# Kernel tuning notes

Measured on AMD Instinct MI355X. Metric: run time of the kernel, lower is better.

## Reference

```python
import jax, jax.numpy as jnp
import numpy as np

N_NODES = 100_000
N_EDGES = 1_600_000
HIDDEN = 128
OUT_DIM = 400


def setup_inputs() -> dict:
    key = jax.random.key(0)
    ks = jax.random.split(key, 6)
    x = jax.random.normal(ks[0], (N_NODES, 1), dtype=jnp.float32)
    edge_index = jax.random.randint(ks[1], (2, N_EDGES), 0, N_NODES, dtype=jnp.int32)
    # Glorot-style init for the two GCN weight matrices
    W1 = jax.random.normal(ks[2], (1, HIDDEN), dtype=jnp.float32) * (1.0 / np.sqrt(1 + HIDDEN))
    b1 = jnp.zeros((HIDDEN,), dtype=jnp.float32)
    W2 = jax.random.normal(ks[3], (HIDDEN, OUT_DIM), dtype=jnp.float32) * (1.0 / np.sqrt(HIDDEN + OUT_DIM))
    b2 = jnp.zeros((OUT_DIM,), dtype=jnp.float32)
    return {"x": x, "edge_index": edge_index, "W1": W1, "b1": b1, "W2": W2, "b2": b2}


def _gcn_layer(x, W, b, row, col, norm, num_nodes):
    # PyG GCNConv: out[col] += norm * (x @ W)[row]; then + bias
    h = x @ W                                   # [N, F_out]
    msg = h[row] * norm[:, None]                # [E+N, F_out] gather + scale
    out = jax.ops.segment_sum(msg, col, num_segments=num_nodes)  # scatter-add
    return out + b


def reference(x, edge_index, W1, b1, W2, b2):
    n = x.shape[0]
    loops = jnp.arange(n, dtype=edge_index.dtype)
    row = jnp.concatenate([edge_index[0], loops])  # sources (+ self loops)
    col = jnp.concatenate([edge_index[1], loops])  # destinations (+ self loops)
    # symmetric normalization: deg over destinations, norm = d^-1/2[row] * d^-1/2[col]
    deg = jnp.zeros((n,), dtype=x.dtype).at[col].add(1.0)  # >=1 due to self loops
    dinv = jax.lax.rsqrt(deg)
    norm = dinv[row] * dinv[col]
    h = jax.nn.relu(_gcn_layer(x, W1, b1, row, col, norm, n))
    h = _gcn_layer(h, W2, b2, row, col, norm, n)
    return h.mean(axis=0)  # [OUT_DIM]
```

## Files before the change

kernel.cpp:

```cpp
#include <hip/hip_runtime.h>
#include <math.h>


constexpr int BKT_BITS = 10;
constexpr int BKT_SIZE = 1 << BKT_BITS;
constexpr int NBMAX    = 128;
constexpr int CAP      = 17408;
constexpr int SLICES   = 8;
constexpr int SLICES_D = 8;
constexpr int EPT      = 8;

__global__ void init_cur(int* __restrict__ curC, int* __restrict__ curR,
                         float* __restrict__ total) {
    int t = threadIdx.x;
    if (t < NBMAX) { curC[t] = t * CAP; curR[t] = t * CAP; }
    if (t < 128) total[t] = 0.0f;
}

__global__ void scatter_edges(const int* __restrict__ row, const int* __restrict__ col,
                              int* __restrict__ SC, int* __restrict__ SR,
                              int* __restrict__ curC, int* __restrict__ curR, int E) {
    __shared__ int hC[NBMAX], hR[NBMAX], bC[NBMAX], bR[NBMAX];
    const int TILE = blockDim.x * EPT;
    const int myBase = blockIdx.x * TILE + threadIdx.x * EPT;
    int r[EPT], c[EPT];
    if (myBase + EPT <= E) {
        int4 r0 = *reinterpret_cast<const int4*>(row + myBase);
        int4 r1 = *reinterpret_cast<const int4*>(row + myBase + 4);
        int4 c0 = *reinterpret_cast<const int4*>(col + myBase);
        int4 c1 = *reinterpret_cast<const int4*>(col + myBase + 4);
        r[0]=r0.x; r[1]=r0.y; r[2]=r0.z; r[3]=r0.w;
        r[4]=r1.x; r[5]=r1.y; r[6]=r1.z; r[7]=r1.w;
        c[0]=c0.x; c[1]=c0.y; c[2]=c0.z; c[3]=c0.w;
        c[4]=c1.x; c[5]=c1.y; c[6]=c1.z; c[7]=c1.w;
    } else {
#pragma unroll
        for (int j = 0; j < EPT; ++j) {
            int e = myBase + j;
            r[j] = (e < E) ? row[e] : -1;
            c[j] = (e < E) ? col[e] : -1;
        }
    }
    if (threadIdx.x < NBMAX) { hC[threadIdx.x] = 0; hR[threadIdx.x] = 0; }
    __syncthreads();
#pragma unroll
    for (int j = 0; j < EPT; ++j) {
        if (r[j] >= 0) {
            atomicAdd(&hC[c[j] >> BKT_BITS], 1);
            atomicAdd(&hR[r[j] >> BKT_BITS], 1);
        }
    }
    __syncthreads();
    if (threadIdx.x < NBMAX) {
        bC[threadIdx.x] = atomicAdd(&curC[threadIdx.x], hC[threadIdx.x]);
        hC[threadIdx.x] = 0;
        bR[threadIdx.x] = atomicAdd(&curR[threadIdx.x], hR[threadIdx.x]);
        hR[threadIdx.x] = 0;
    }
    __syncthreads();
#pragma unroll
    for (int j = 0; j < EPT; ++j) {
        if (r[j] >= 0) {
            int kb = c[j] >> BKT_BITS;
            int idx = bC[kb] + atomicAdd(&hC[kb], 1);
            if (idx < (kb + 1) * CAP)
                SC[idx] = ((c[j] & (BKT_SIZE - 1)) << 17) | r[j];
            int kb2 = r[j] >> BKT_BITS;
            int idx2 = bR[kb2] + atomicAdd(&hR[kb2], 1);
            if (idx2 < (kb2 + 1) * CAP)
                SR[idx2] = ((r[j] & (BKT_SIZE - 1)) << 17) | c[j];
        }
    }
}

__global__ void hist_deg(const int* __restrict__ SC, const int* __restrict__ cur,
                         float* __restrict__ P, int stride) {
    __shared__ float bins[BKT_SIZE];
    const int b = blockIdx.x / SLICES_D, s = blockIdx.x % SLICES_D;
    const int base = b * CAP;
    int len = cur[b] - base;
    len = len < CAP ? len : CAP;
    const int lo = base + (int)((long long)len * s / SLICES_D);
    const int hi = base + (int)((long long)len * (s + 1) / SLICES_D);
    for (int i = threadIdx.x; i < BKT_SIZE; i += blockDim.x) bins[i] = 0.0f;
    __syncthreads();
    for (int e = lo + threadIdx.x; e < hi; e += blockDim.x)
        atomicAdd(&bins[SC[e] >> 17], 1.0f);
    __syncthreads();
    float* dst = P + (size_t)s * stride + b * BKT_SIZE;
    for (int i = threadIdx.x; i < BKT_SIZE; i += blockDim.x) dst[i] = bins[i];
}

__global__ void finalize_deg(const float* __restrict__ Pd, const float* __restrict__ x,
                             float* __restrict__ dinv, float* __restrict__ u,
                             int N, int stride) {
    int i = blockIdx.x * blockDim.x + threadIdx.x;
    if (i >= N) return;
    float d = 1.0f;
#pragma unroll
    for (int s = 0; s < SLICES_D; ++s) d += Pd[(size_t)s * stride + i];
    float di = rsqrtf(d);
    dinv[i] = di;
    u[i] = di * x[i];
}

__global__ void hist_gather_both(const int* __restrict__ SC, const int* __restrict__ SR,
                                 const int* __restrict__ curC, const int* __restrict__ curR,
                                 const float* __restrict__ u, const float* __restrict__ dinv,
                                 float* __restrict__ Ps, float* __restrict__ Pw,
                                 int stride, int half) {
    __shared__ float bins[BKT_SIZE];
    const bool isW = blockIdx.x >= half;
    const int id = isW ? blockIdx.x - half : blockIdx.x;
    const int* S = isW ? SR : SC;
    const int* cur = isW ? curR : curC;
    const float* val = isW ? dinv : u;
    float* P = isW ? Pw : Ps;
    const int b = id / SLICES, s = id % SLICES;
    const int base = b * CAP;
    int len = cur[b] - base;
    len = len < CAP ? len : CAP;
    const int lo = base + (int)((long long)len * s / SLICES);
    const int hi = base + (int)((long long)len * (s + 1) / SLICES);
    for (int i = threadIdx.x; i < BKT_SIZE; i += blockDim.x) bins[i] = 0.0f;
    __syncthreads();
    for (int e = lo + threadIdx.x; e < hi; e += blockDim.x) {
        int v = S[e];
        atomicAdd(&bins[v >> 17], val[v & 0x1FFFF]);
    }
    __syncthreads();
    float* dst = P + (size_t)s * stride + b * BKT_SIZE;
    for (int i = threadIdx.x; i < BKT_SIZE; i += blockDim.x) dst[i] = bins[i];
}

__global__ void fused_node(const float* __restrict__ Ps, const float* __restrict__ Pw,
                           const float* __restrict__ dinv, const float* __restrict__ x,
                           const float* __restrict__ W1, const float* __restrict__ b1,
                           float* __restrict__ total, int N, int stride) {
    __shared__ float scs[256];
    __shared__ float ws[256];
    __shared__ float red[256];
    const int tid = threadIdx.x;
    const int i = blockIdx.x * 256 + tid;
    float scv = 0.0f, wv = 0.0f;
    if (i < N) {
        float sr = 0.0f, wr = 0.0f;
#pragma unroll
        for (int s = 0; s < SLICES; ++s) {
            sr += Ps[(size_t)s * stride + i];
            wr += Pw[(size_t)s * stride + i];
        }
        float di = dinv[i];
        scv = di * sr + di * di * x[i];
        wv  = di * (wr + di);
    }
    scs[tid] = scv;
    ws[tid]  = wv;
    __syncthreads();
    const int k = tid & 127;
    const int base = (tid >> 7) * 128;
    const float w1k = W1[k];
    const float b1k = b1[k];
    float acc = 0.0f;
#pragma unroll 4
    for (int j = 0; j < 128; ++j) {
        float h = scs[base + j] * w1k + b1k;
        h = h > 0.0f ? h : 0.0f;
        acc += ws[base + j] * h;
    }
    red[tid] = acc;
    __syncthreads();
    if (tid < 128)
        atomicAdd(&total[k], red[tid] + red[tid + 128]);
}

__global__ void final_out(const float* __restrict__ total,
                          const float* __restrict__ W2, const float* __restrict__ b2,
                          float* __restrict__ out, int OUT, float invN) {
    __shared__ float t[128];
    const int tid = threadIdx.x;
    if (tid < 128) t[tid] = total[tid] * invN;
    __syncthreads();
    const int d = blockIdx.x * 128 + tid;
    if (d < OUT) {
        float acc = b2[d];
#pragma unroll 4
        for (int kk = 0; kk < 128; ++kk) acc += t[kk] * W2[kk * OUT + d];
        out[d] = acc;
    }
}

extern "C" void kernel_launch(void* const* d_in, const int* in_sizes, int n_in,
                              void* d_out, int out_size, void* d_ws, size_t ws_size,
                              hipStream_t stream) {
    const float* x          = (const float*)d_in[0];
    const int*   edge_index = (const int*)  d_in[1];
    const float* W1         = (const float*)d_in[2];
    const float* b1         = (const float*)d_in[3];
    const float* W2         = (const float*)d_in[4];
    const float* b2         = (const float*)d_in[5];
    float* out = (float*)d_out;

    const int N   = in_sizes[0];
    const int E   = in_sizes[1] / 2;
    const int OUT = in_sizes[5];

    const int* row = edge_index;
    const int* col = edge_index + E;

    const int NB = (N + BKT_SIZE - 1) >> BKT_BITS;
    const int stride = NB * BKT_SIZE;

    char* p = (char*)d_ws;
    float* dinv  = (float*)p; p += (size_t)N * 4;
    float* u     = (float*)p; p += (size_t)N * 4;
    float* total = (float*)p; p += 512;
    int*   ints  = (int*)p;   p += 1024;
    int*   SC    = (int*)p;   p += (size_t)NB * CAP * 4;
    int*   SR    = (int*)p;   p += (size_t)NB * CAP * 4;
    float* P     = (float*)p;
    float* Ps    = P;
    float* Pw    = P + (size_t)SLICES * stride;

    int* curC = ints;
    int* curR = ints + NBMAX;

    const int TILE = 256 * EPT;
    const int nTiles = (E + TILE - 1) / TILE;

    init_cur<<<1, 256, 0, stream>>>(curC, curR, total);
    scatter_edges<<<nTiles, 256, 0, stream>>>(row, col, SC, SR, curC, curR, E);
    hist_deg<<<NB * SLICES_D, 256, 0, stream>>>(SC, curC, P, stride);
    finalize_deg<<<(N + 255) / 256, 256, 0, stream>>>(P, x, dinv, u, N, stride);
    const int half = NB * SLICES;
    hist_gather_both<<<2 * half, 256, 0, stream>>>(SC, SR, curC, curR, u, dinv,
                                                   Ps, Pw, stride, half);
    fused_node<<<(N + 255) / 256, 256, 0, stream>>>(Ps, Pw, dinv, x, W1, b1,
                                                    total, N, stride);
    final_out<<<(OUT + 127) / 128, 128, 0, stream>>>(total, W2, b2, out, OUT,
                                                     1.0f / (float)N);
}
```

Before: 168.9 us.

## Fuse GCN pipeline into one cooperative persistent kernel with grid syncs

Replaces the six separate kernel launches with a single cooperative kernel of 512 persistent blocks that runs each stage in grid-stride loops, separated by grid.sync(). Histogram stages now give each bucket to one block, with vectorised int4 reads, instead of splitting it into 8 slices with partial buffers, so the slice reduction passes are gone. The aim is to remove per-launch overhead and partial-sum traffic. The costs are grid-wide barrier latency and less parallelism in the histogram stages, since there are only about 98 buckets per pass (about 196 tasks in the combined gather stage), well below 512 blocks.

```diff
diff --git a/kernel.cpp b/kernel.cpp
--- a/kernel.cpp
+++ b/kernel.cpp
@@ -1,242 +1,248 @@
 #include <hip/hip_runtime.h>
+#include <hip/hip_cooperative_groups.h>
 #include <math.h>
+
+namespace cg = cooperative_groups;
 
 
 constexpr int BKT_BITS = 10;
 constexpr int BKT_SIZE = 1 << BKT_BITS;
-constexpr int NBMAX    = 128;
+constexpr int NBP      = 128;
 constexpr int CAP      = 17408;
-constexpr int SLICES   = 8;
-constexpr int SLICES_D = 8;
 constexpr int EPT      = 8;
+constexpr int TPB      = 256;
+constexpr int GRID     = 512;
 
 __global__ void init_cur(int* __restrict__ curC, int* __restrict__ curR,
                          float* __restrict__ total) {
     int t = threadIdx.x;
-    if (t < NBMAX) { curC[t] = t * CAP; curR[t] = t * CAP; }
+    if (t < NBP) { curC[t] = t * CAP; curR[t] = t * CAP; }
     if (t < 128) total[t] = 0.0f;
 }
 
-__global__ void scatter_edges(const int* __restrict__ row, const int* __restrict__ col,
-                              int* __restrict__ SC, int* __restrict__ SR,
-                              int* __restrict__ curC, int* __restrict__ curR, int E) {
-    __shared__ int hC[NBMAX], hR[NBMAX], bC[NBMAX], bR[NBMAX];
-    const int TILE = blockDim.x * EPT;
-    const int myBase = blockIdx.x * TILE + threadIdx.x * EPT;
-    int r[EPT], c[EPT];
-    if (myBase + EPT <= E) {
-        int4 r0 = *reinterpret_cast<const int4*>(row + myBase);
-        int4 r1 = *reinterpret_cast<const int4*>(row + myBase + 4);
-        int4 c0 = *reinterpret_cast<const int4*>(col + myBase);
-        int4 c1 = *reinterpret_cast<const int4*>(col + myBase + 4);
-        r[0]=r0.x; r[1]=r0.y; r[2]=r0.z; r[3]=r0.w;
-        r[4]=r1.x; r[5]=r1.y; r[6]=r1.z; r[7]=r1.w;
-        c[0]=c0.x; c[1]=c0.y; c[2]=c0.z; c[3]=c0.w;
-        c[4]=c1.x; c[5]=c1.y; c[6]=c1.z; c[7]=c1.w;
-    } else {
+__global__ __launch_bounds__(TPB, 4)
+void gcn_mono(const int* __restrict__ row, const int* __restrict__ col,
+              const float* __restrict__ x,
+              const float* __restrict__ W1, const float* __restrict__ b1,
+              const float* __restrict__ W2, const float* __restrict__ b2,
+              int* __restrict__ SC, int* __restrict__ SR,
+              int* __restrict__ curC, int* __restrict__ curR,
+              float* __restrict__ dinv, float* __restrict__ u,
+              float* __restrict__ s_raw, float* __restrict__ w_raw,
+              float* __restrict__ total, float* __restrict__ out,
+              int N, int E, int NB, int OUT) {
+    cg::grid_group grid = cg::this_grid();
+    __shared__ int hC[NBP], hR[NBP], bC[NBP], bR[NBP];
+    __shared__ float bins[BKT_SIZE];
+    __shared__ float scs[TPB], ws[TPB], red[TPB];
+    const int tid = threadIdx.x;
+
+    const int TILE = TPB * EPT;
+    const int nTiles = (E + TILE - 1) / TILE;
+    for (int t = blockIdx.x; t < nTiles; t += gridDim.x) {
+        const int myBase = t * TILE + tid * EPT;
+        int r[EPT], c[EPT];
+        if (myBase + EPT <= E) {
+            int4 r0 = *reinterpret_cast<const int4*>(row + myBase);
+            int4 r1 = *reinterpret_cast<const int4*>(row + myBase + 4);
+            int4 c0 = *reinterpret_cast<const int4*>(col + myBase);
+            int4 c1 = *reinterpret_cast<const int4*>(col + myBase + 4);
+            r[0]=r0.x; r[1]=r0.y; r[2]=r0.z; r[3]=r0.w;
+            r[4]=r1.x; r[5]=r1.y; r[6]=r1.z; r[7]=r1.w;
+            c[0]=c0.x; c[1]=c0.y; c[2]=c0.z; c[3]=c0.w;
+            c[4]=c1.x; c[5]=c1.y; c[6]=c1.z; c[7]=c1.w;
+        } else {
+#pragma unroll
+            for (int j = 0; j < EPT; ++j) {
+                int e = myBase + j;
+                r[j] = (e < E) ? row[e] : -1;
+                c[j] = (e < E) ? col[e] : -1;
+            }
+        }
+        if (tid < NBP) { hC[tid] = 0; hR[tid] = 0; }
+        __syncthreads();
 #pragma unroll
         for (int j = 0; j < EPT; ++j) {
-            int e = myBase + j;
-            r[j] = (e < E) ? row[e] : -1;
-            c[j] = (e < E) ? col[e] : -1;
-        }
-    }
-    if (threadIdx.x < NBMAX) { hC[threadIdx.x] = 0; hR[threadIdx.x] = 0; }
-    __syncthreads();
+            if (r[j] >= 0) {
+                atomicAdd(&hC[c[j] >> BKT_BITS], 1);
+                atomicAdd(&hR[r[j] >> BKT_BITS], 1);
+            }
+        }
+        __syncthreads();
+        if (tid < NBP) {
+            bC[tid] = atomicAdd(&curC[tid], hC[tid]);
+            hC[tid] = 0;
+            bR[tid] = atomicAdd(&curR[tid], hR[tid]);
+            hR[tid] = 0;
+        }
+        __syncthreads();
 #pragma unroll
-    for (int j = 0; j < EPT; ++j) {
-        if (r[j] >= 0) {
-            atomicAdd(&hC[c[j] >> BKT_BITS], 1);
-            atomicAdd(&hR[r[j] >> BKT_BITS], 1);
-        }
-    }
-    __syncthreads();
-    if (threadIdx.x < NBMAX) {
-        bC[threadIdx.x] = atomicAdd(&curC[threadIdx.x], hC[threadIdx.x]);
-        hC[threadIdx.x] = 0;
-        bR[threadIdx.x] = atomicAdd(&curR[threadIdx.x], hR[threadIdx.x]);
-        hR[threadIdx.x] = 0;
-    }
-    __syncthreads();
-#pragma unroll
-    for (int j = 0; j < EPT; ++j) {
-        if (r[j] >= 0) {
-            int kb = c[j] >> BKT_BITS;
-            int idx = bC[kb] + atomicAdd(&hC[kb], 1);
-            if (idx < (kb + 1) * CAP)
-                SC[idx] = ((c[j] & (BKT_SIZE - 1)) << 17) | r[j];
-            int kb2 = r[j] >> BKT_BITS;
-            int idx2 = bR[kb2] + atomicAdd(&hR[kb2], 1);
-            if (idx2 < (kb2 + 1) * CAP)
-                SR[idx2] = ((r[j] & (BKT_SIZE - 1)) << 17) | c[j];
-        }
-    }
-}
-
-__global__ void hist_deg(const int* __restrict__ SC, const int* __restrict__ cur,
-                         float* __restrict__ P, int stride) {
-    __shared__ float bins[BKT_SIZE];
-    const int b = blockIdx.x / SLICES_D, s = blockIdx.x % SLICES_D;
-    const int base = b * CAP;
-    int len = cur[b] - base;
-    len = len < CAP ? len : CAP;
-    const int lo = base + (int)((long long)len * s / SLICES_D);
-    const int hi = base + (int)((long long)len * (s + 1) / SLICES_D);
-    for (int i = threadIdx.x; i < BKT_SIZE; i += blockDim.x) bins[i] = 0.0f;
-    __syncthreads();
-    for (int e = lo + threadIdx.x; e < hi; e += blockDim.x)
-        atomicAdd(&bins[SC[e] >> 17], 1.0f);
-    __syncthreads();
-    float* dst = P + (size_t)s * stride + b * BKT_SIZE;
-    for (int i = threadIdx.x; i < BKT_SIZE; i += blockDim.x) dst[i] = bins[i];
-}
-
-__global__ void finalize_deg(const float* __restrict__ Pd, const float* __restrict__ x,
-                             float* __restrict__ dinv, float* __restrict__ u,
-                             int N, int stride) {
-    int i = blockIdx.x * blockDim.x + threadIdx.x;
-    if (i >= N) return;
-    float d = 1.0f;
-#pragma unroll
-    for (int s = 0; s < SLICES_D; ++s) d += Pd[(size_t)s * stride + i];
-    float di = rsqrtf(d);
-    dinv[i] = di;
-    u[i] = di * x[i];
-}
-
-__global__ void hist_gather_both(const int* __restrict__ SC, const int* __restrict__ SR,
-                                 const int* __restrict__ curC, const int* __restrict__ curR,
-                                 const float* __restrict__ u, const float* __restrict__ dinv,
-                                 float* __restrict__ Ps, float* __restrict__ Pw,
-                                 int stride, int half) {
-    __shared__ float bins[BKT_SIZE];
-    const bool isW = blockIdx.x >= half;
-    const int id = isW ? blockIdx.x - half : blockIdx.x;
-    const int* S = isW ? SR : SC;
-    const int* cur = isW ? curR : curC;
-    const float* val = isW ? dinv : u;
-    float* P = isW ? Pw : Ps;
-    const int b = id / SLICES, s = id % SLICES;
-    const int base = b * CAP;
-    int len = cur[b] - base;
-    len = len < CAP ? len : CAP;
-    const int lo = base + (int)((long long)len * s / SLICES);
-    const int hi = base + (int)((long long)len * (s + 1) / SLICES);
-    for (int i = threadIdx.x; i < BKT_SIZE; i += blockDim.x) bins[i] = 0.0f;
-    __syncthreads();
-    for (int e = lo + threadIdx.x; e < hi; e += blockDim.x) {
-        int v = S[e];
-        atomicAdd(&bins[v >> 17], val[v & 0x1FFFF]);
-    }
-    __syncthreads();
-    float* dst = P + (size_t)s * stride + b * BKT_SIZE;
-    for (int i = threadIdx.x; i < BKT_SIZE; i += blockDim.x) dst[i] = bins[i];
-}
-
-__global__ void fused_node(const float* __restrict__ Ps, const float* __restrict__ Pw,
-                           const float* __restrict__ dinv, const float* __restrict__ x,
-                           const float* __restrict__ W1, const float* __restrict__ b1,
-                           float* __restrict__ total, int N, int stride) {
-    __shared__ float scs[256];
-    __shared__ float ws[256];
-    __shared__ float red[256];
-    const int tid = threadIdx.x;
-    const int i = blockIdx.x * 256 + tid;
-    float scv = 0.0f, wv = 0.0f;
-    if (i < N) {
-        float sr = 0.0f, wr = 0.0f;
-#pragma unroll
-        for (int s = 0; s < SLICES; ++s) {
-            sr += Ps[(size_t)s * stride + i];
-            wr += Pw[(size_t)s * stride + i];
-        }
-        float di = dinv[i];
-        scv = di * sr + di * di * x[i];
-        wv  = di * (wr + di);
-    }
-    scs[tid] = scv;
-    ws[tid]  = wv;
-    __syncthreads();
+        for (int j = 0; j < EPT; ++j) {
+            if (r[j] >= 0) {
+                int kb = c[j] >> BKT_BITS;
+                int idx = bC[kb] + atomicAdd(&hC[kb], 1);
+                if (idx < (kb + 1) * CAP)
+                    SC[idx] = ((c[j] & (BKT_SIZE - 1)) << 17) | r[j];
+                int kb2 = r[j] >> BKT_BITS;
+                int idx2 = bR[kb2] + atomicAdd(&hR[kb2], 1);
+                if (idx2 < (kb2 + 1) * CAP)
+                    SR[idx2] = ((r[j] & (BKT_SIZE - 1)) << 17) | c[j];
+            }
+        }
+        __syncthreads();
+    }
+    grid.sync();
+
+    for (int b = blockIdx.x; b < NB; b += gridDim.x) {
+        for (int i = tid; i < BKT_SIZE; i += TPB) bins[i] = 0.0f;
+        __syncthreads();
+        const int base = b * CAP;
+        int len = curC[b] - base;
+        len = len < CAP ? len : CAP;
+        const int nv = len >> 2;
+        for (int q = tid; q < nv; q += TPB) {
+            int4 v = reinterpret_cast<const int4*>(SC + base)[q];
+            atomicAdd(&bins[v.x >> 17], 1.0f);
+            atomicAdd(&bins[v.y >> 17], 1.0f);
+            atomicAdd(&bins[v.z >> 17], 1.0f);
+            atomicAdd(&bins[v.w >> 17], 1.0f);
+        }
+        for (int e = base + (nv << 2) + tid; e < base + len; e += TPB)
+            atomicAdd(&bins[SC[e] >> 17], 1.0f);
+        __syncthreads();
+        const int lo = b * BKT_SIZE;
+        for (int i = tid; i < BKT_SIZE; i += TPB) {
+            int node = lo + i;
+            if (node < N) {
+                float di = rsqrtf(1.0f + bins[i]);
+                dinv[node] = di;
+                u[node] = di * x[node];
+            }
+        }
+        __syncthreads();
+    }
+    grid.sync();
+
+    for (int tsk = blockIdx.x; tsk < 2 * NB; tsk += gridDim.x) {
+        const bool isW = tsk >= NB;
+        const int b = isW ? tsk - NB : tsk;
+        const int* S = isW ? SR : SC;
+        const int* cur = isW ? curR : curC;
+        const float* val = isW ? dinv : u;
+        float* dst = isW ? w_raw : s_raw;
+        for (int i = tid; i < BKT_SIZE; i += TPB) bins[i] = 0.0f;
+        __syncthreads();
+        const int base = b * CAP;
+        int len = cur[b] - base;
+        len = len < CAP ? len : CAP;
+        const int nv = len >> 2;
+        for (int q = tid; q < nv; q += TPB) {
+            int4 v = reinterpret_cast<const int4*>(S + base)[q];
+            float a0 = val[v.x & 0x1FFFF];
+            float a1 = val[v.y & 0x1FFFF];
+            float a2 = val[v.z & 0x1FFFF];
+            float a3 = val[v.w & 0x1FFFF];
+            atomicAdd(&bins[v.x >> 17], a0);
+            atomicAdd(&bins[v.y >> 17], a1);
+            atomicAdd(&bins[v.z >> 17], a2);
+            atomicAdd(&bins[v.w >> 17], a3);
+        }
+        for (int e = base + (nv << 2) + tid; e < base + len; e += TPB) {
+            int v = S[e];
+            atomicAdd(&bins[v >> 17], val[v & 0x1FFFF]);
+        }
+        __syncthreads();
+        float* d = dst + b * BKT_SIZE;
+        for (int i = tid; i < BKT_SIZE; i += TPB) d[i] = bins[i];
+        __syncthreads();
+    }
+    grid.sync();
+
     const int k = tid & 127;
-    const int base = (tid >> 7) * 128;
+    const int kbase = (tid >> 7) * 128;
     const float w1k = W1[k];
     const float b1k = b1[k];
     float acc = 0.0f;
+    const int nChunk = (N + TPB - 1) / TPB;
+    for (int chunk = blockIdx.x; chunk < nChunk; chunk += gridDim.x) {
+        const int i = chunk * TPB + tid;
+        float scv = 0.0f, wv = 0.0f;
+        if (i < N) {
+            float di = dinv[i];
+            scv = di * s_raw[i] + di * di * x[i];
+            wv  = di * (w_raw[i] + di);
+        }
+        scs[tid] = scv;
+        ws[tid]  = wv;
+        __syncthreads();
 #pragma unroll 4
-    for (int j = 0; j < 128; ++j) {
-        float h = scs[base + j] * w1k + b1k;
-        h = h > 0.0f ? h : 0.0f;
-        acc += ws[base + j] * h;
+        for (int j = 0; j < 128; ++j) {
+            float h = scs[kbase + j] * w1k + b1k;
+            h = h > 0.0f ? h : 0.0f;
+            acc += ws[kbase + j] * h;
+        }
+        __syncthreads();
     }
     red[tid] = acc;
     __syncthreads();
-    if (tid < 128)
-        atomicAdd(&total[k], red[tid] + red[tid + 128]);
-}
-
-__global__ void final_out(const float* __restrict__ total,
-                          const float* __restrict__ W2, const float* __restrict__ b2,
-                          float* __restrict__ out, int OUT, float invN) {
-    __shared__ float t[128];
-    const int tid = threadIdx.x;
-    if (tid < 128) t[tid] = total[tid] * invN;
-    __syncthreads();
-    const int d = blockIdx.x * 128 + tid;
-    if (d < OUT) {
-        float acc = b2[d];
+    if (tid < 128) atomicAdd(&total[tid], red[tid] + red[tid + 128]);
+    grid.sync();
+
+    const float invN = 1.0f / (float)N;
+    for (int d0 = blockIdx.x * TPB; d0 < OUT; d0 += gridDim.x * TPB) {
+        if (tid < 128) red[tid] = total[tid] * invN;
+        __syncthreads();
+        const int d = d0 + tid;
+        if (d < OUT) {
+            float a = b2[d];
 #pragma unroll 4
-        for (int kk = 0; kk < 128; ++kk) acc += t[kk] * W2[kk * OUT + d];
-        out[d] = acc;
+            for (int kk = 0; kk < 128; ++kk) a += red[kk] * W2[kk * OUT + d];
+            out[d] = a;
+        }
+        __syncthreads();
     }
 }
 
 extern "C" void kernel_launch(void* const* d_in, const int* in_sizes, int n_in,
                               void* d_out, int out_size, void* d_ws, size_t ws_size,
                               hipStream_t stream) {
-    const float* x          = (const float*)d_in[0];
-    const int*   edge_index = (const int*)  d_in[1];
-    const float* W1         = (const float*)d_in[2];
-    const float* b1         = (const float*)d_in[3];
-    const float* W2         = (const float*)d_in[4];
-    const float* b2         = (const float*)d_in[5];
+    const int* row    = (const int*)  d_in[1];
+    const float* x    = (const float*)d_in[0];
+    const float* W1   = (const float*)d_in[2];
+    const float* b1   = (const float*)d_in[3];
+    const float* W2   = (const float*)d_in[4];
+    const float* b2   = (const float*)d_in[5];
     float* out = (float*)d_out;
 
-    const int N   = in_sizes[0];
-    const int E   = in_sizes[1] / 2;
-    const int OUT = in_sizes[5];
-
-    const int* row = edge_index;
-    const int* col = edge_index + E;
-
-    const int NB = (N + BKT_SIZE - 1) >> BKT_BITS;
+    int N   = in_sizes[0];
+    int E   = in_sizes[1] / 2;
+    int OUT = in_sizes[5];
+    const int* col = row + E;
+
+    int NB = (N + BKT_SIZE - 1) >> BKT_BITS;
     const int stride = NB * BKT_SIZE;
 
     char* p = (char*)d_ws;
     float* dinv  = (float*)p; p += (size_t)N * 4;
     float* u     = (float*)p; p += (size_t)N * 4;
+    float* s_raw = (float*)p; p += (size_t)stride * 4;
+    float* w_raw = (float*)p; p += (size_t)stride * 4;
     float* total = (float*)p; p += 512;
-    int*   ints  = (int*)p;   p += 1024;
+    int*   curC  = (int*)p;   p += NBP * 4;
+    int*   curR  = (int*)p;   p += NBP * 4;
     int*   SC    = (int*)p;   p += (size_t)NB * CAP * 4;
-    int*   SR    = (int*)p;   p += (size_t)NB * CAP * 4;
-    float* P     = (float*)p;
-    float* Ps    = P;
-    float* Pw    = P + (size_t)SLICES * stride;
-
-    int* curC = ints;
-    int* curR = ints + NBMAX;
-
-    const int TILE = 256 * EPT;
-    const int nTiles = (E + TILE - 1) / TILE;
+    int*   SR    = (int*)p;
 
     init_cur<<<1, 256, 0, stream>>>(curC, curR, total);
-    scatter_edges<<<nTiles, 256, 0, stream>>>(row, col, SC, SR, curC, curR, E);
-    hist_deg<<<NB * SLICES_D, 256, 0, stream>>>(SC, curC, P, stride);
-    finalize_deg<<<(N + 255) / 256, 256, 0, stream>>>(P, x, dinv, u, N, stride);
-    const int half = NB * SLICES;
-    hist_gather_both<<<2 * half, 256, 0, stream>>>(SC, SR, curC, curR, u, dinv,
-                                                   Ps, Pw, stride, half);
-    fused_node<<<(N + 255) / 256, 256, 0, stream>>>(Ps, Pw, dinv, x, W1, b1,
-                                                    total, N, stride);
-    final_out<<<(OUT + 127) / 128, 128, 0, stream>>>(total, W2, b2, out, OUT,
-                                                     1.0f / (float)N);
+
+    void* args[] = {
+        (void*)&row, (void*)&col, (void*)&x,
+        (void*)&W1, (void*)&b1, (void*)&W2, (void*)&b2,
+        (void*)&SC, (void*)&SR, (void*)&curC, (void*)&curR,
+        (void*)&dinv, (void*)&u, (void*)&s_raw, (void*)&w_raw,
+        (void*)&total, (void*)&out,
+        (void*)&N, (void*)&E, (void*)&NB, (void*)&OUT
+    };
+    hipLaunchCooperativeKernel((const void*)gcn_mono, dim3(GRID), dim3(TPB),
+                               args, 0, stream);
 }
```

After: 387.0 us. +129.2%, slower.

## Fuse degree finalize into histogram via last-block pattern, vectorize bucket reads

Applied to the files above, without the earlier changes.

Merges the degree histogram and the degree finalize step into one kernel: the last slice block of each bucket, chosen by an atomic done counter, sums the per-slice partials and writes dinv and u. The init kernel becomes a memset, which makes the bucket cursors relative offsets. Bucket reads in the histogram and gather kernels now use int4 loads with a scalar tail. The partial buffers move to a bucket-major layout so the slices of one bucket sit next to each other. This removes one launch and one pass over the partials, at the cost of threadfences and a serialized last-block reduction. Ps aliases Pd, which the gather kernel overwrites after the degree kernel has consumed it.

```diff
diff --git a/kernel.cpp b/kernel.cpp
--- a/kernel.cpp
+++ b/kernel.cpp
@@ -4,24 +4,19 @@
 
 constexpr int BKT_BITS = 10;
 constexpr int BKT_SIZE = 1 << BKT_BITS;
-constexpr int NBMAX    = 128;
+constexpr int NBP      = 128;
 constexpr int CAP      = 17408;
+constexpr int SLICES_D = 8;
 constexpr int SLICES   = 8;
-constexpr int SLICES_D = 8;
 constexpr int EPT      = 8;
-
-__global__ void init_cur(int* __restrict__ curC, int* __restrict__ curR,
-                         float* __restrict__ total) {
-    int t = threadIdx.x;
-    if (t < NBMAX) { curC[t] = t * CAP; curR[t] = t * CAP; }
-    if (t < 128) total[t] = 0.0f;
-}
-
-__global__ void scatter_edges(const int* __restrict__ row, const int* __restrict__ col,
-                              int* __restrict__ SC, int* __restrict__ SR,
-                              int* __restrict__ curC, int* __restrict__ curR, int E) {
-    __shared__ int hC[NBMAX], hR[NBMAX], bC[NBMAX], bR[NBMAX];
-    const int TILE = blockDim.x * EPT;
+constexpr int TPB      = 256;
+
+__global__ __launch_bounds__(TPB)
+void scatter_edges(const int* __restrict__ row, const int* __restrict__ col,
+                   int* __restrict__ SC, int* __restrict__ SR,
+                   int* __restrict__ curC, int* __restrict__ curR, int E) {
+    __shared__ int hC[NBP], hR[NBP], bC[NBP], bR[NBP];
+    const int TILE = TPB * EPT;
     const int myBase = blockIdx.x * TILE + threadIdx.x * EPT;
     int r[EPT], c[EPT];
     if (myBase + EPT <= E) {
@@ -41,7 +36,7 @@
             c[j] = (e < E) ? col[e] : -1;
         }
     }
-    if (threadIdx.x < NBMAX) { hC[threadIdx.x] = 0; hR[threadIdx.x] = 0; }
+    if (threadIdx.x < NBP) { hC[threadIdx.x] = 0; hR[threadIdx.x] = 0; }
     __syncthreads();
 #pragma unroll
     for (int j = 0; j < EPT; ++j) {
@@ -51,7 +46,7 @@
         }
     }
     __syncthreads();
-    if (threadIdx.x < NBMAX) {
+    if (threadIdx.x < NBP) {
         bC[threadIdx.x] = atomicAdd(&curC[threadIdx.x], hC[threadIdx.x]);
         hC[threadIdx.x] = 0;
         bR[threadIdx.x] = atomicAdd(&curR[threadIdx.x], hR[threadIdx.x]);
@@ -62,53 +57,73 @@
     for (int j = 0; j < EPT; ++j) {
         if (r[j] >= 0) {
             int kb = c[j] >> BKT_BITS;
-            int idx = bC[kb] + atomicAdd(&hC[kb], 1);
-            if (idx < (kb + 1) * CAP)
-                SC[idx] = ((c[j] & (BKT_SIZE - 1)) << 17) | r[j];
+            int loc = bC[kb] + atomicAdd(&hC[kb], 1);
+            if (loc < CAP)
+                SC[kb * CAP + loc] = ((c[j] & (BKT_SIZE - 1)) << 17) | r[j];
             int kb2 = r[j] >> BKT_BITS;
-            int idx2 = bR[kb2] + atomicAdd(&hR[kb2], 1);
-            if (idx2 < (kb2 + 1) * CAP)
-                SR[idx2] = ((r[j] & (BKT_SIZE - 1)) << 17) | c[j];
-        }
-    }
-}
-
-__global__ void hist_deg(const int* __restrict__ SC, const int* __restrict__ cur,
-                         float* __restrict__ P, int stride) {
+            int loc2 = bR[kb2] + atomicAdd(&hR[kb2], 1);
+            if (loc2 < CAP)
+                SR[kb2 * CAP + loc2] = ((r[j] & (BKT_SIZE - 1)) << 17) | c[j];
+        }
+    }
+}
+
+__global__ __launch_bounds__(TPB)
+void hist_deg_fin(const int* __restrict__ SC, const int* __restrict__ curC,
+                  float* __restrict__ Pd, int* __restrict__ doneD,
+                  const float* __restrict__ x,
+                  float* __restrict__ dinv, float* __restrict__ u, int N) {
     __shared__ float bins[BKT_SIZE];
+    __shared__ int amLast;
     const int b = blockIdx.x / SLICES_D, s = blockIdx.x % SLICES_D;
+    const int tid = threadIdx.x;
+    for (int i = tid; i < BKT_SIZE; i += TPB) bins[i] = 0.0f;
+    __syncthreads();
     const int base = b * CAP;
-    int len = cur[b] - base;
+    int len = curC[b];
     len = len < CAP ? len : CAP;
-    const int lo = base + (int)((long long)len * s / SLICES_D);
-    const int hi = base + (int)((long long)len * (s + 1) / SLICES_D);
-    for (int i = threadIdx.x; i < BKT_SIZE; i += blockDim.x) bins[i] = 0.0f;
-    __syncthreads();
-    for (int e = lo + threadIdx.x; e < hi; e += blockDim.x)
-        atomicAdd(&bins[SC[e] >> 17], 1.0f);
-    __syncthreads();
-    float* dst = P + (size_t)s * stride + b * BKT_SIZE;
-    for (int i = threadIdx.x; i < BKT_SIZE; i += blockDim.x) dst[i] = bins[i];
-}
-
-__global__ void finalize_deg(const float* __restrict__ Pd, const float* __restrict__ x,
-                             float* __restrict__ dinv, float* __restrict__ u,
-                             int N, int stride) {
-    int i = blockIdx.x * blockDim.x + threadIdx.x;
-    if (i >= N) return;
-    float d = 1.0f;
-#pragma unroll
-    for (int s = 0; s < SLICES_D; ++s) d += Pd[(size_t)s * stride + i];
-    float di = rsqrtf(d);
-    dinv[i] = di;
-    u[i] = di * x[i];
-}
-
-__global__ void hist_gather_both(const int* __restrict__ SC, const int* __restrict__ SR,
-                                 const int* __restrict__ curC, const int* __restrict__ curR,
-                                 const float* __restrict__ u, const float* __restrict__ dinv,
-                                 float* __restrict__ Ps, float* __restrict__ Pw,
-                                 int stride, int half) {
+    const int nv = len >> 2;
+    const int q0 = (int)((long long)nv * s / SLICES_D);
+    const int q1 = (int)((long long)nv * (s + 1) / SLICES_D);
+    const int4* SC4 = reinterpret_cast<const int4*>(SC + base);
+    for (int q = q0 + tid; q < q1; q += TPB) {
+        int4 v = SC4[q];
+        atomicAdd(&bins[v.x >> 17], 1.0f);
+        atomicAdd(&bins[v.y >> 17], 1.0f);
+        atomicAdd(&bins[v.z >> 17], 1.0f);
+        atomicAdd(&bins[v.w >> 17], 1.0f);
+    }
+    if (s == SLICES_D - 1)
+        for (int e = base + (nv << 2) + tid; e < base + len; e += TPB)
+            atomicAdd(&bins[SC[e] >> 17], 1.0f);
+    __syncthreads();
+    float* dst = Pd + ((size_t)b * SLICES_D + s) * BKT_SIZE;
+    for (int i = tid; i < BKT_SIZE; i += TPB) dst[i] = bins[i];
+    __threadfence();
+    __syncthreads();
+    if (tid == 0) amLast = (atomicAdd(&doneD[b], 1) == SLICES_D - 1);
+    __syncthreads();
+    if (!amLast) return;
+    __threadfence();
+    const float* src = Pd + (size_t)b * SLICES_D * BKT_SIZE;
+    for (int i = tid; i < BKT_SIZE; i += TPB) {
+        float d = 1.0f;
+#pragma unroll
+        for (int s2 = 0; s2 < SLICES_D; ++s2) d += src[s2 * BKT_SIZE + i];
+        int node = b * BKT_SIZE + i;
+        if (node < N) {
+            float di = rsqrtf(d);
+            dinv[node] = di;
+            u[node] = di * x[node];
+        }
+    }
+}
+
+__global__ __launch_bounds__(TPB)
+void gather_both(const int* __restrict__ SC, const int* __restrict__ SR,
+                 const int* __restrict__ curC, const int* __restrict__ curR,
+                 const float* __restrict__ u, const float* __restrict__ dinv,
+                 float* __restrict__ Ps, float* __restrict__ Pw, int half) {
     __shared__ float bins[BKT_SIZE];
     const bool isW = blockIdx.x >= half;
     const int id = isW ? blockIdx.x - half : blockIdx.x;
@@ -117,38 +132,58 @@
     const float* val = isW ? dinv : u;
     float* P = isW ? Pw : Ps;
     const int b = id / SLICES, s = id % SLICES;
+    const int tid = threadIdx.x;
+    for (int i = tid; i < BKT_SIZE; i += TPB) bins[i] = 0.0f;
+    __syncthreads();
     const int base = b * CAP;
-    int len = cur[b] - base;
+    int len = cur[b];
     len = len < CAP ? len : CAP;
-    const int lo = base + (int)((long long)len * s / SLICES);
-    const int hi = base + (int)((long long)len * (s + 1) / SLICES);
-    for (int i = threadIdx.x; i < BKT_SIZE; i += blockDim.x) bins[i] = 0.0f;
-    __syncthreads();
-    for (int e = lo + threadIdx.x; e < hi; e += blockDim.x) {
-        int v = S[e];
-        atomicAdd(&bins[v >> 17], val[v & 0x1FFFF]);
-    }
-    __syncthreads();
-    float* dst = P + (size_t)s * stride + b * BKT_SIZE;
-    for (int i = threadIdx.x; i < BKT_SIZE; i += blockDim.x) dst[i] = bins[i];
-}
-
-__global__ void fused_node(const float* __restrict__ Ps, const float* __restrict__ Pw,
-                           const float* __restrict__ dinv, const float* __restrict__ x,
-                           const float* __restrict__ W1, const float* __restrict__ b1,
-                           float* __restrict__ total, int N, int stride) {
-    __shared__ float scs[256];
-    __shared__ float ws[256];
-    __shared__ float red[256];
-    const int tid = threadIdx.x;
-    const int i = blockIdx.x * 256 + tid;
+    const int nv = len >> 2;
+    const int q0 = (int)((long long)nv * s / SLICES);
+    const int q1 = (int)((long long)nv * (s + 1) / SLICES);
+    const int4* S4 = reinterpret_cast<const int4*>(S + base);
+    for (int q = q0 + tid; q < q1; q += TPB) {
+        int4 v = S4[q];
+        float a0 = val[v.x & 0x1FFFF];
+        float a1 = val[v.y & 0x1FFFF];
+        float a2 = val[v.z & 0x1FFFF];
+        float a3 = val[v.w & 0x1FFFF];
+        atomicAdd(&bins[v.x >> 17], a0);
+        atomicAdd(&bins[v.y >> 17], a1);
+        atomicAdd(&bins[v.z >> 17], a2);
+        atomicAdd(&bins[v.w >> 17], a3);
+    }
+    if (s == SLICES - 1)
+        for (int e = base + (nv << 2) + tid; e < base + len; e += TPB) {
+            int v = S[e];
+            atomicAdd(&bins[v >> 17], val[v & 0x1FFFF]);
+        }
+    __syncthreads();
+    float* dst = P + ((size_t)b * SLICES + s) * BKT_SIZE;
+    for (int i = tid; i < BKT_SIZE; i += TPB) dst[i] = bins[i];
+}
+
+__global__ __launch_bounds__(TPB)
+void fused_node(const float* __restrict__ Ps, const float* __restrict__ Pw,
+                const float* __restrict__ dinv, const float* __restrict__ x,
+                const float* __restrict__ W1, const float* __restrict__ b1,
+                float* __restrict__ total, int N) {
+    __shared__ float scs[TPB];
+    __shared__ float ws[TPB];
+    __shared__ float red[TPB];
+    const int tid = threadIdx.x;
+    const int i = blockIdx.x * TPB + tid;
     float scv = 0.0f, wv = 0.0f;
     if (i < N) {
+        const size_t pb = (size_t)(i >> BKT_BITS);
+        const int idx = i & (BKT_SIZE - 1);
+        const float* ps = Ps + pb * SLICES * BKT_SIZE + idx;
+        const float* pw = Pw + pb * SLICES * BKT_SIZE + idx;
         float sr = 0.0f, wr = 0.0f;
 #pragma unroll
         for (int s = 0; s < SLICES; ++s) {
-            sr += Ps[(size_t)s * stride + i];
-            wr += Pw[(size_t)s * stride + i];
+            sr += ps[s * BKT_SIZE];
+            wr += pw[s * BKT_SIZE];
         }
         float di = dinv[i];
         scv = di * sr + di * di * x[i];
@@ -158,15 +193,15 @@
     ws[tid]  = wv;
     __syncthreads();
     const int k = tid & 127;
-    const int base = (tid >> 7) * 128;
+    const int kbase = (tid >> 7) * 128;
     const float w1k = W1[k];
     const float b1k = b1[k];
     float acc = 0.0f;
 #pragma unroll 4
     for (int j = 0; j < 128; ++j) {
-        float h = scs[base + j] * w1k + b1k;
+        float h = scs[kbase + j] * w1k + b1k;
         h = h > 0.0f ? h : 0.0f;
-        acc += ws[base + j] * h;
+        acc += ws[kbase + j] * h;
     }
     red[tid] = acc;
     __syncthreads();
@@ -174,12 +209,13 @@
         atomicAdd(&total[k], red[tid] + red[tid + 128]);
 }
 
-__global__ void final_out(const float* __restrict__ total,
-                          const float* __restrict__ W2, const float* __restrict__ b2,
-                          float* __restrict__ out, int OUT, float invN) {
+__global__ __launch_bounds__(128)
+void final_out(const float* __restrict__ total,
+               const float* __restrict__ W2, const float* __restrict__ b2,
+               float* __restrict__ out, int OUT, float invN) {
     __shared__ float t[128];
     const int tid = threadIdx.x;
-    if (tid < 128) t[tid] = total[tid] * invN;
+    t[tid] = total[tid] * invN;
     __syncthreads();
     const int d = blockIdx.x * 128 + tid;
     if (d < OUT) {
@@ -193,50 +229,47 @@
 extern "C" void kernel_launch(void* const* d_in, const int* in_sizes, int n_in,
                               void* d_out, int out_size, void* d_ws, size_t ws_size,
                               hipStream_t stream) {
-    const float* x          = (const float*)d_in[0];
-    const int*   edge_index = (const int*)  d_in[1];
-    const float* W1         = (const float*)d_in[2];
-    const float* b1         = (const float*)d_in[3];
-    const float* W2         = (const float*)d_in[4];
-    const float* b2         = (const float*)d_in[5];
+    const float* x  = (const float*)d_in[0];
+    const int* row  = (const int*)  d_in[1];
+    const float* W1 = (const float*)d_in[2];
+    const float* b1 = (const float*)d_in[3];
+    const float* W2 = (const float*)d_in[4];
+    const float* b2 = (const float*)d_in[5];
     float* out = (float*)d_out;
 
     const int N   = in_sizes[0];
     const int E   = in_sizes[1] / 2;
     const int OUT = in_sizes[5];
-
-    const int* row = edge_index;
-    const int* col = edge_index + E;
+    const int* col = row + E;
 
     const int NB = (N + BKT_SIZE - 1) >> BKT_BITS;
-    const int stride = NB * BKT_SIZE;
 
     char* p = (char*)d_ws;
     float* dinv  = (float*)p; p += (size_t)N * 4;
     float* u     = (float*)p; p += (size_t)N * 4;
-    float* total = (float*)p; p += 512;
-    int*   ints  = (int*)p;   p += 1024;
+    int*   ints  = (int*)p;   p += 384 * 4;
+    float* total = (float*)p; p += 128 * 4;
     int*   SC    = (int*)p;   p += (size_t)NB * CAP * 4;
     int*   SR    = (int*)p;   p += (size_t)NB * CAP * 4;
-    float* P     = (float*)p;
-    float* Ps    = P;
-    float* Pw    = P + (size_t)SLICES * stride;
-
-    int* curC = ints;
-    int* curR = ints + NBMAX;
-
-    const int TILE = 256 * EPT;
-    const int nTiles = (E + TILE - 1) / TILE;
-
-    init_cur<<<1, 256, 0, stream>>>(curC, curR, total);
-    scatter_edges<<<nTiles, 256, 0, stream>>>(row, col, SC, SR, curC, curR, E);
-    hist_deg<<<NB * SLICES_D, 256, 0, stream>>>(SC, curC, P, stride);
-    finalize_deg<<<(N + 255) / 256, 256, 0, stream>>>(P, x, dinv, u, N, stride);
+    float* Pd    = (float*)p; p += (size_t)NB * SLICES_D * BKT_SIZE * 4;
+    float* Ps    = Pd;
+    float* Pw    = (float*)p;
+
+    int* curC  = ints;
+    int* curR  = ints + NBP;
+    int* doneD = ints + 2 * NBP;
+
+    hipMemsetAsync(ints, 0, 384 * 4 + 128 * 4, stream);
+
+    const int nTiles = (E + TPB * EPT - 1) / (TPB * EPT);
+    scatter_edges<<<nTiles, TPB, 0, stream>>>(row, col, SC, SR, curC, curR, E);
+    hist_deg_fin<<<NB * SLICES_D, TPB, 0, stream>>>(SC, curC, Pd, doneD,
+                                                    x, dinv, u, N);
     const int half = NB * SLICES;
-    hist_gather_both<<<2 * half, 256, 0, stream>>>(SC, SR, curC, curR, u, dinv,
-                                                   Ps, Pw, stride, half);
-    fused_node<<<(N + 255) / 256, 256, 0, stream>>>(Ps, Pw, dinv, x, W1, b1,
-                                                    total, N, stride);
+    gather_both<<<2 * half, TPB, 0, stream>>>(SC, SR, curC, curR, u, dinv,
+                                              Ps, Pw, half);
+    fused_node<<<(N + TPB - 1) / TPB, TPB, 0, stream>>>(Ps, Pw, dinv, x,
+                                                        W1, b1, total, N);
     final_out<<<(OUT + 127) / 128, 128, 0, stream>>>(total, W2, b2, out, OUT,
                                                      1.0f / (float)N);
 }
```

New measurement: 265.4 us. 1.57x slower.
